# Kernel tuning notes

Measured on AMD Instinct MI355X. Metric: run time of the kernel, lower is better.

Reference implementation:

```python
import jax, jax.numpy as jnp
import numpy as np

BLOCK_SIZE = 64
IN_CHANNELS = 1024
OUT_CHANNELS = 1024
O_NBLOCKS = OUT_CHANNELS // BLOCK_SIZE  # 16
I_NBLOCKS = IN_CHANNELS // BLOCK_SIZE   # 16
N_TOKENS = 32768


def setup_inputs() -> dict:
    key = jax.random.key(0)
    kx, kw = jax.random.split(key)
    x = jax.random.normal(kx, (N_TOKENS, IN_CHANNELS), dtype=jnp.float32)
    # xavier_uniform over the (o_nblocks, i_nblocks, block_size) tensor:
    # fan_in = i_nblocks * block_size, fan_out = block_size (last-dim convention)
    fan_in = I_NBLOCKS * BLOCK_SIZE
    fan_out = BLOCK_SIZE
    limit = float(np.sqrt(6.0 / (fan_in + fan_out)))
    w = jax.random.uniform(kw, (O_NBLOCKS, I_NBLOCKS, BLOCK_SIZE),
                           dtype=jnp.float32, minval=-limit, maxval=limit)
    return {"x": x, "w": w}


def _build_dense_weight(w):
    # w: (R, Q, bs). Dense W[r*bs+i, q*bs+j] = w[r, q, (i - j) mod bs]
    R, Q, bs = w.shape
    i = jnp.arange(bs)
    idx = (i[:, None] - i[None, :]) % bs          # (bs, bs) circulant index
    Wb = w[:, :, idx]                              # (R, Q, bs, bs)
    return Wb.transpose(0, 2, 1, 3).reshape(R * bs, Q * bs)  # (out, in)


def reference(x, w):
    W = _build_dense_weight(w)                     # (out_channels, in_channels)
    return x @ W.T                                 # F.linear, no bias
```

## Files before the change

kernel.cpp:

```cpp
#include <hip/hip_runtime.h>
#include <stdint.h>


#define NTOK 32768
#define NCH  1024
#define BK   64
#define NKT  (NCH / BK)

typedef short bf16x8 __attribute__((ext_vector_type(8)));
typedef float f32x4  __attribute__((ext_vector_type(4)));
typedef unsigned short u16x8 __attribute__((ext_vector_type(8)));

static __device__ __forceinline__ unsigned short f2bf(float f) {
    unsigned int u = __float_as_uint(f);
    u += 0x7FFFu + ((u >> 16) & 1u);
    return (unsigned short)(u >> 16);
}

#define GLOAD16(gp, lp)                                                          \
    __builtin_amdgcn_global_load_lds(                                            \
        (const __attribute__((address_space(1))) unsigned int*)(gp),             \
        (__attribute__((address_space(3))) unsigned int*)(lp), 16, 0, 0)

__global__ void cvt_x_kernel(const float* __restrict__ x, unsigned short* __restrict__ xb) {
    int i = blockIdx.x * blockDim.x + threadIdx.x;
    int row = i >> 7;
    int j   = i & 127;
    const float4* src = (const float4*)(x + (((size_t)row) << 10) + (j << 3));
    float4 a = src[0], b = src[1];
    u16x8 v;
    v[0]=f2bf(a.x); v[1]=f2bf(a.y); v[2]=f2bf(a.z); v[3]=f2bf(a.w);
    v[4]=f2bf(b.x); v[5]=f2bf(b.y); v[6]=f2bf(b.z); v[7]=f2bf(b.w);
    int js = (j & ~7) | ((j & 7) ^ (row & 7));
    *(u16x8*)(xb + (((size_t)row) << 10) + (js << 3)) = v;
}

__global__ void build_w_kernel(const float* __restrict__ w, unsigned short* __restrict__ Wb) {
    int i = blockIdx.x * blockDim.x + threadIdx.x;
    int o = i >> 7;
    int j = i & 127;
    int r = o >> 6;
    int q = j >> 3;
    const float* wrow = w + ((r * 16 + q) << 6);
    int k0 = j << 3;
    u16x8 v;
#pragma unroll
    for (int e = 0; e < 8; ++e) v[e] = f2bf(wrow[(o - (k0 + e)) & 63]);
    int js = (j & ~7) | ((j & 7) ^ (o & 7));
    *(u16x8*)(Wb + (((size_t)o) << 10) + (js << 3)) = v;
}

#define PHASE_BAR() __builtin_amdgcn_s_barrier()
#define LGKM0() asm volatile("s_waitcnt lgkmcnt(0)" ::: "memory")
#define VMCNT0() asm volatile("s_waitcnt vmcnt(0)" ::: "memory")
#define SETPRIO(n) __builtin_amdgcn_s_setprio(n)
#define MFMA4(d, av, bv) d = __builtin_amdgcn_mfma_f32_16x16x32_bf16(av, bv, d, 0, 0, 0)
#define NOHOOK ((void)0)

#define STAGE(bufA, bufB, t) do {                                                \
    const char* _sa = srcA + ((t) << 7);                                         \
    const char* _sb = srcB + ((t) << 7);                                         \
    char* _da = (bufA) + (wv << 10);                                             \
    char* _db = (bufB) + (wv << 10);                                             \
    GLOAD16(_sa, _da); GLOAD16(_sa + (64 << 11), _da + 8192);                    \
    GLOAD16(_sb, _db); GLOAD16(_sb + (64 << 11), _db + 8192);                    \
} while (0)

#define KSTEP(Abuf, Bbuf, DO_STAGE) do {                                         \
    DO_STAGE;                                                                    \
    bf16x8 afr[4][2], bfr[2][2];                                                 \
    _Pragma("unroll") for (int m = 0; m < 4; ++m)                                \
      _Pragma("unroll") for (int ks = 0; ks < 2; ++ks)                           \
        afr[m][ks] = *(const bf16x8*)((Abuf) + a_off[ks] + m * 2048);            \
    _Pragma("unroll") for (int n = 0; n < 2; ++n)                                \
      _Pragma("unroll") for (int ks = 0; ks < 2; ++ks)                           \
        bfr[n][ks] = *(const bf16x8*)((Bbuf) + b_off[ks] + n * 2048);            \
    LGKM0();                                                                     \
    SETPRIO(1);                                                                  \
    _Pragma("unroll") for (int m = 0; m < 4; ++m)                                \
      _Pragma("unroll") for (int n = 0; n < 2; ++n) {                            \
        MFMA4(acc[m][n], afr[m][0], bfr[n][0]);                                  \
        MFMA4(acc[m][n], afr[m][1], bfr[n][1]);                                  \
      }                                                                          \
    SETPRIO(0);                                                                  \
} while (0)

__global__ void __launch_bounds__(512, 4) gemm128_kernel(const unsigned short* __restrict__ A,
                                                         const unsigned short* __restrict__ B,
                                                         float* __restrict__ C) {
    __shared__ __align__(16) char lds[65536];
    char* As0 = lds;
    char* As1 = lds + 16384;
    char* Bs0 = lds + 32768;
    char* Bs1 = lds + 49152;

    int tid  = threadIdx.x;
    int lane = tid & 63;
    int wv   = tid >> 6;
    int wr   = wv >> 2;
    int wc   = wv & 3;

    int cpx = gridDim.x >> 3;
    int wid = ((int)blockIdx.x & 7) * cpx + ((int)blockIdx.x >> 3);
    int tn = wid & 7, tm = wid >> 3;
    int m0 = tm * 128, n0 = tn * 128;

    const char* srcA = (const char*)A + (((size_t)(m0 + (tid >> 3))) << 11) + ((tid & 7) << 4);
    const char* srcB = (const char*)B + (((size_t)(n0 + (tid >> 3))) << 11) + ((tid & 7) << 4);

    int xa   = (lane & 7) << 4;
    int kq16 = (lane >> 4) << 4;
    int abase = (wr * 64 + (lane & 15)) * 128;
    int bbase = (wc * 32 + (lane & 15)) * 128;
    int a_off[2] = { abase + (kq16 ^ xa), abase + ((64 + kq16) ^ xa) };
    int b_off[2] = { bbase + (kq16 ^ xa), bbase + ((64 + kq16) ^ xa) };

    f32x4 acc[4][2] = {};

    STAGE(As0, Bs0, 0);
    VMCNT0(); PHASE_BAR();

    for (int t = 0; t < NKT; t += 2) {
        KSTEP(As0, Bs0, STAGE(As1, Bs1, t + 1));
        VMCNT0(); PHASE_BAR();
        if (t + 2 < NKT) {
            KSTEP(As1, Bs1, STAGE(As0, Bs0, t + 2));
            VMCNT0(); PHASE_BAR();
        } else {
            KSTEP(As1, Bs1, NOHOOK);
        }
    }

    float* Cp = C + ((size_t)(m0 + wr * 64)) * NCH + n0 + wc * 32;
    int cc = lane & 15;
    int rr = (lane >> 4) << 2;
#pragma unroll
    for (int m = 0; m < 4; ++m)
#pragma unroll
        for (int j = 0; j < 4; ++j) {
            float* rowp = Cp + ((size_t)(m * 16 + rr + j)) * NCH;
#pragma unroll
            for (int n = 0; n < 2; ++n)
                rowp[n * 16 + cc] = acc[m][n][j];
        }
}

__global__ void naive_kernel(const float* __restrict__ x, const float* __restrict__ w,
                             float* __restrict__ out) {
    int t = blockIdx.x;
    int o = blockIdx.y * 256 + threadIdx.x;
    const float* xr = x + (size_t)t * NCH;
    int r = o >> 6, oi = o & 63;
    float s = 0.f;
    for (int q = 0; q < 16; ++q) {
        const float* wq = w + (r * 16 + q) * 64;
        const float* xq = xr + q * 64;
#pragma unroll 8
        for (int j = 0; j < 64; ++j) s += xq[j] * wq[(oi - j) & 63];
    }
    out[(size_t)t * NCH + o] = s;
}

extern "C" void kernel_launch(void* const* d_in, const int* in_sizes, int n_in,
                              void* d_out, int out_size, void* d_ws, size_t ws_size,
                              hipStream_t stream) {
    const float* x = (const float*)d_in[0];
    const float* w = (const float*)d_in[1];
    float* out = (float*)d_out;

    const size_t needX = (size_t)NTOK * NCH * sizeof(unsigned short);
    const size_t needW = (size_t)NCH * NCH * sizeof(unsigned short);

    if (ws_size >= needX + needW) {
        unsigned short* xb = (unsigned short*)d_ws;
        unsigned short* Wb = (unsigned short*)((char*)d_ws + needX);
        hipLaunchKernelGGL(cvt_x_kernel, dim3(NTOK * 128 / 256), dim3(256), 0, stream, x, xb);
        hipLaunchKernelGGL(build_w_kernel, dim3(NCH * 128 / 256), dim3(256), 0, stream, w, Wb);
        hipLaunchKernelGGL(gemm128_kernel, dim3(2048), dim3(512), 0, stream, xb, Wb, out);
    } else {
        hipLaunchKernelGGL(naive_kernel, dim3(NTOK, 4), dim3(256), 0, stream, x, w, out);
    }
}
```

Measured before the change: 111.4 us.

## Fuse fp32-to-bf16 conversion of x into the GEMM A-tile loading

Drops the separate conversion pass that wrote a bf16 copy of x. The GEMM now loads fp32 x tiles into registers, converts them to bf16 and writes them to LDS in the swizzled layout, while B still streams directly to LDS. This saves a full read and write pass over the activations, but it doubles the A bytes fetched per tile, and each A tile is re-read by every column tile. The register staging also adds VALU work and vmcnt waits to the main loop.

```diff
diff --git a/kernel.cpp b/kernel.cpp
--- a/kernel.cpp
+++ b/kernel.cpp
@@ -17,23 +17,17 @@
     return (unsigned short)(u >> 16);
 }
 
+static __device__ __forceinline__ u16x8 pack8(float4 a, float4 b) {
+    u16x8 v;
+    v[0]=f2bf(a.x); v[1]=f2bf(a.y); v[2]=f2bf(a.z); v[3]=f2bf(a.w);
+    v[4]=f2bf(b.x); v[5]=f2bf(b.y); v[6]=f2bf(b.z); v[7]=f2bf(b.w);
+    return v;
+}
+
 #define GLOAD16(gp, lp)                                                          \
     __builtin_amdgcn_global_load_lds(                                            \
         (const __attribute__((address_space(1))) unsigned int*)(gp),             \
         (__attribute__((address_space(3))) unsigned int*)(lp), 16, 0, 0)
-
-__global__ void cvt_x_kernel(const float* __restrict__ x, unsigned short* __restrict__ xb) {
-    int i = blockIdx.x * blockDim.x + threadIdx.x;
-    int row = i >> 7;
-    int j   = i & 127;
-    const float4* src = (const float4*)(x + (((size_t)row) << 10) + (j << 3));
-    float4 a = src[0], b = src[1];
-    u16x8 v;
-    v[0]=f2bf(a.x); v[1]=f2bf(a.y); v[2]=f2bf(a.z); v[3]=f2bf(a.w);
-    v[4]=f2bf(b.x); v[5]=f2bf(b.y); v[6]=f2bf(b.z); v[7]=f2bf(b.w);
-    int js = (j & ~7) | ((j & 7) ^ (row & 7));
-    *(u16x8*)(xb + (((size_t)row) << 10) + (js << 3)) = v;
-}
 
 __global__ void build_w_kernel(const float* __restrict__ w, unsigned short* __restrict__ Wb) {
     int i = blockIdx.x * blockDim.x + threadIdx.x;
@@ -52,22 +46,32 @@
 
 #define PHASE_BAR() __builtin_amdgcn_s_barrier()
 #define LGKM0() asm volatile("s_waitcnt lgkmcnt(0)" ::: "memory")
-#define VMCNT0() asm volatile("s_waitcnt vmcnt(0)" ::: "memory")
+#define VMCNT(n) asm volatile("s_waitcnt vmcnt(" #n ")" ::: "memory")
+#define CFENCE() asm volatile("" ::: "memory")
 #define SETPRIO(n) __builtin_amdgcn_s_setprio(n)
 #define MFMA4(d, av, bv) d = __builtin_amdgcn_mfma_f32_16x16x32_bf16(av, bv, d, 0, 0, 0)
-#define NOHOOK ((void)0)
 
-#define STAGE(bufA, bufB, t) do {                                                \
-    const char* _sa = srcA + ((t) << 7);                                         \
-    const char* _sb = srcB + ((t) << 7);                                         \
-    char* _da = (bufA) + (wv << 10);                                             \
-    char* _db = (bufB) + (wv << 10);                                             \
-    GLOAD16(_sa, _da); GLOAD16(_sa + (64 << 11), _da + 8192);                    \
-    GLOAD16(_sb, _db); GLOAD16(_sb + (64 << 11), _db + 8192);                    \
+#define ISSUE_A(t) do {                                                          \
+    const float4* _p = (const float4*)(pA + ((t) << 6));                         \
+    areg[0] = _p[0]; areg[1] = _p[1]; areg[2] = _p[2]; areg[3] = _p[3];          \
+    CFENCE();                                                                    \
 } while (0)
 
-#define KSTEP(Abuf, Bbuf, DO_STAGE) do {                                         \
-    DO_STAGE;                                                                    \
+#define WRITE_A(Abuf) do {                                                       \
+    u16x8 _w0 = pack8(areg[0], areg[1]);                                         \
+    u16x8 _w1 = pack8(areg[2], areg[3]);                                         \
+    *(u16x8*)((Abuf) + aw0) = _w0;                                               \
+    *(u16x8*)((Abuf) + aw1) = _w1;                                               \
+    CFENCE();                                                                    \
+} while (0)
+
+#define STAGE_B(buf, t) do {                                                     \
+    const char* _s = srcB + ((t) << 7);                                          \
+    char* _d = (buf) + (wv << 10);                                               \
+    GLOAD16(_s, _d); GLOAD16(_s + (64 << 11), _d + 8192);                        \
+} while (0)
+
+#define KCOMPUTE(Abuf, Bbuf) do {                                                \
     bf16x8 afr[4][2], bfr[2][2];                                                 \
     _Pragma("unroll") for (int m = 0; m < 4; ++m)                                \
       _Pragma("unroll") for (int ks = 0; ks < 2; ++ks)                           \
@@ -85,9 +89,9 @@
     SETPRIO(0);                                                                  \
 } while (0)
 
-__global__ void __launch_bounds__(512, 4) gemm128_kernel(const unsigned short* __restrict__ A,
-                                                         const unsigned short* __restrict__ B,
-                                                         float* __restrict__ C) {
+__global__ void __launch_bounds__(512, 4) gemm_fused_kernel(const float* __restrict__ X,
+                                                            const unsigned short* __restrict__ B,
+                                                            float* __restrict__ C) {
     __shared__ __align__(16) char lds[65536];
     char* As0 = lds;
     char* As1 = lds + 16384;
@@ -105,7 +109,15 @@
     int tn = wid & 7, tm = wid >> 3;
     int m0 = tm * 128, n0 = tn * 128;
 
-    const char* srcA = (const char*)A + (((size_t)(m0 + (tid >> 3))) << 11) + ((tid & 7) << 4);
+    const float* pA = X + ((size_t)(m0 + (tid >> 2)) << 10) + ((tid & 3) << 4);
+    float4 areg[4];
+
+    int wrow = tid >> 2;
+    int j0   = (tid & 3) << 1;
+    int r7   = wrow & 7;
+    int aw0  = wrow * 128 + (((j0    ) ^ r7) << 4);
+    int aw1  = wrow * 128 + (((j0 + 1) ^ r7) << 4);
+
     const char* srcB = (const char*)B + (((size_t)(n0 + (tid >> 3))) << 11) + ((tid & 7) << 4);
 
     int xa   = (lane & 7) << 4;
@@ -117,17 +129,24 @@
 
     f32x4 acc[4][2] = {};
 
-    STAGE(As0, Bs0, 0);
-    VMCNT0(); PHASE_BAR();
+    ISSUE_A(0); STAGE_B(Bs0, 0);
+    VMCNT(2);
+    WRITE_A(As0);
+    VMCNT(0); LGKM0();
+    PHASE_BAR();
 
     for (int t = 0; t < NKT; t += 2) {
-        KSTEP(As0, Bs0, STAGE(As1, Bs1, t + 1));
-        VMCNT0(); PHASE_BAR();
+        ISSUE_A(t + 1); STAGE_B(Bs1, t + 1);
+        KCOMPUTE(As0, Bs0);
+        VMCNT(2); WRITE_A(As1);
+        VMCNT(0); LGKM0(); PHASE_BAR();
         if (t + 2 < NKT) {
-            KSTEP(As1, Bs1, STAGE(As0, Bs0, t + 2));
-            VMCNT0(); PHASE_BAR();
+            ISSUE_A(t + 2); STAGE_B(Bs0, t + 2);
+            KCOMPUTE(As1, Bs1);
+            VMCNT(2); WRITE_A(As0);
+            VMCNT(0); LGKM0(); PHASE_BAR();
         } else {
-            KSTEP(As1, Bs1, NOHOOK);
+            KCOMPUTE(As1, Bs1);
         }
     }
 
@@ -168,15 +187,12 @@
     const float* w = (const float*)d_in[1];
     float* out = (float*)d_out;
 
-    const size_t needX = (size_t)NTOK * NCH * sizeof(unsigned short);
     const size_t needW = (size_t)NCH * NCH * sizeof(unsigned short);
 
-    if (ws_size >= needX + needW) {
-        unsigned short* xb = (unsigned short*)d_ws;
-        unsigned short* Wb = (unsigned short*)((char*)d_ws + needX);
-        hipLaunchKernelGGL(cvt_x_kernel, dim3(NTOK * 128 / 256), dim3(256), 0, stream, x, xb);
+    if (ws_size >= needW) {
+        unsigned short* Wb = (unsigned short*)d_ws;
         hipLaunchKernelGGL(build_w_kernel, dim3(NCH * 128 / 256), dim3(256), 0, stream, w, Wb);
-        hipLaunchKernelGGL(gemm128_kernel, dim3(2048), dim3(512), 0, stream, xb, Wb, out);
+        hipLaunchKernelGGL(gemm_fused_kernel, dim3(2048), dim3(512), 0, stream, x, Wb, out);
     } else {
         hipLaunchKernelGGL(naive_kernel, dim3(NTOK, 4), dim3(256), 0, stream, x, w, out);
     }
```

New measurement: 115.3 us. 3.5% more time.

## Deepen GEMM LDS pipeline to keep two k-tiles of loads in flight

Applied to the files above, without the earlier changes.

Restructures the main GEMM loop so that two k-tiles are staged ahead. Each step reads its fragments, barriers, then reissues the async global-to-LDS load into the same buffer it just consumed. The step ends with a partial vmcnt wait that only requires the older tile to have landed. This is meant to hide global load latency better than the previous wait-for-all-loads pattern, at the cost of an extra barrier per k-step and a longer unrolled tail.

```diff
diff --git a/kernel.cpp b/kernel.cpp
--- a/kernel.cpp
+++ b/kernel.cpp
@@ -4,8 +4,7 @@
 
 #define NTOK 32768
 #define NCH  1024
-#define BK   64
-#define NKT  (NCH / BK)
+#define NKT  16
 
 typedef short bf16x8 __attribute__((ext_vector_type(8)));
 typedef float f32x4  __attribute__((ext_vector_type(4)));
@@ -50,9 +49,9 @@
     *(u16x8*)(Wb + (((size_t)o) << 10) + (js << 3)) = v;
 }
 
-#define PHASE_BAR() __builtin_amdgcn_s_barrier()
+#define BAR() __builtin_amdgcn_s_barrier()
 #define LGKM0() asm volatile("s_waitcnt lgkmcnt(0)" ::: "memory")
-#define VMCNT0() asm volatile("s_waitcnt vmcnt(0)" ::: "memory")
+#define VMCNT(n) asm volatile("s_waitcnt vmcnt(" #n ")" ::: "memory")
 #define SETPRIO(n) __builtin_amdgcn_s_setprio(n)
 #define MFMA4(d, av, bv) d = __builtin_amdgcn_mfma_f32_16x16x32_bf16(av, bv, d, 0, 0, 0)
 #define NOHOOK ((void)0)
@@ -66,8 +65,7 @@
     GLOAD16(_sb, _db); GLOAD16(_sb + (64 << 11), _db + 8192);                    \
 } while (0)
 
-#define KSTEP(Abuf, Bbuf, DO_STAGE) do {                                         \
-    DO_STAGE;                                                                    \
+#define KSTEP2(Abuf, Bbuf, DO_STAGE, WN) do {                                    \
     bf16x8 afr[4][2], bfr[2][2];                                                 \
     _Pragma("unroll") for (int m = 0; m < 4; ++m)                                \
       _Pragma("unroll") for (int ks = 0; ks < 2; ++ks)                           \
@@ -76,6 +74,8 @@
       _Pragma("unroll") for (int ks = 0; ks < 2; ++ks)                           \
         bfr[n][ks] = *(const bf16x8*)((Bbuf) + b_off[ks] + n * 2048);            \
     LGKM0();                                                                     \
+    BAR();                                                                       \
+    DO_STAGE;                                                                    \
     SETPRIO(1);                                                                  \
     _Pragma("unroll") for (int m = 0; m < 4; ++m)                                \
       _Pragma("unroll") for (int n = 0; n < 2; ++n) {                            \
@@ -83,6 +83,8 @@
         MFMA4(acc[m][n], afr[m][1], bfr[n][1]);                                  \
       }                                                                          \
     SETPRIO(0);                                                                  \
+    WN;                                                                          \
+    BAR();                                                                       \
 } while (0)
 
 __global__ void __launch_bounds__(512, 4) gemm128_kernel(const unsigned short* __restrict__ A,
@@ -118,17 +120,38 @@
     f32x4 acc[4][2] = {};
 
     STAGE(As0, Bs0, 0);
-    VMCNT0(); PHASE_BAR();
-
-    for (int t = 0; t < NKT; t += 2) {
-        KSTEP(As0, Bs0, STAGE(As1, Bs1, t + 1));
-        VMCNT0(); PHASE_BAR();
-        if (t + 2 < NKT) {
-            KSTEP(As1, Bs1, STAGE(As0, Bs0, t + 2));
-            VMCNT0(); PHASE_BAR();
-        } else {
-            KSTEP(As1, Bs1, NOHOOK);
-        }
+    STAGE(As1, Bs1, 1);
+    VMCNT(4); BAR();
+
+    for (int t = 0; t < 12; t += 2) {
+        KSTEP2(As0, Bs0, STAGE(As0, Bs0, t + 2), VMCNT(4));
+        KSTEP2(As1, Bs1, STAGE(As1, Bs1, t + 3), VMCNT(4));
+    }
+    KSTEP2(As0, Bs0, STAGE(As0, Bs0, 14), VMCNT(4));
+    KSTEP2(As1, Bs1, STAGE(As1, Bs1, 15), VMCNT(4));
+    KSTEP2(As0, Bs0, NOHOOK, VMCNT(0));
+    {
+        bf16x8 afr[4][2], bfr[2][2];
+#pragma unroll
+        for (int m = 0; m < 4; ++m)
+#pragma unroll
+            for (int ks = 0; ks < 2; ++ks)
+                afr[m][ks] = *(const bf16x8*)(As1 + a_off[ks] + m * 2048);
+#pragma unroll
+        for (int n = 0; n < 2; ++n)
+#pragma unroll
+            for (int ks = 0; ks < 2; ++ks)
+                bfr[n][ks] = *(const bf16x8*)(Bs1 + b_off[ks] + n * 2048);
+        LGKM0();
+        SETPRIO(1);
+#pragma unroll
+        for (int m = 0; m < 4; ++m)
+#pragma unroll
+            for (int n = 0; n < 2; ++n) {
+                MFMA4(acc[m][n], afr[m][0], bfr[n][0]);
+                MFMA4(acc[m][n], afr[m][1], bfr[n][1]);
+            }
+        SETPRIO(0);
     }
 
     float* Cp = C + ((size_t)(m0 + wr * 64)) * NCH + n0 + wc * 32;
```

After: 109.5 us. No clear change (-1.7%).

## Load B fragments directly from global into registers, dropping B LDS staging

Applied to the files above, without the earlier changes.

The GEMM now fetches the weight (B) fragments straight from global memory into double-buffered registers instead of staging them through LDS. LDS use is halved and the B-side LDS reads are removed, with the weight matrix stored unswizzled so the direct loads line up. This trades LDS traffic and footprint for more global/L2 loads per wave, since each wave row duplicates B fetches, and for higher register pressure.

```diff
diff --git a/kernel.cpp b/kernel.cpp
--- a/kernel.cpp
+++ b/kernel.cpp
@@ -4,8 +4,7 @@
 
 #define NTOK 32768
 #define NCH  1024
-#define BK   64
-#define NKT  (NCH / BK)
+#define NKT  16
 
 typedef short bf16x8 __attribute__((ext_vector_type(8)));
 typedef float f32x4  __attribute__((ext_vector_type(4)));
@@ -46,41 +45,42 @@
     u16x8 v;
 #pragma unroll
     for (int e = 0; e < 8; ++e) v[e] = f2bf(wrow[(o - (k0 + e)) & 63]);
-    int js = (j & ~7) | ((j & 7) ^ (o & 7));
-    *(u16x8*)(Wb + (((size_t)o) << 10) + (js << 3)) = v;
+    *(u16x8*)(Wb + (((size_t)o) << 10) + (j << 3)) = v;
 }
 
-#define PHASE_BAR() __builtin_amdgcn_s_barrier()
+#define BAR() __builtin_amdgcn_s_barrier()
 #define LGKM0() asm volatile("s_waitcnt lgkmcnt(0)" ::: "memory")
 #define VMCNT0() asm volatile("s_waitcnt vmcnt(0)" ::: "memory")
 #define SETPRIO(n) __builtin_amdgcn_s_setprio(n)
 #define MFMA4(d, av, bv) d = __builtin_amdgcn_mfma_f32_16x16x32_bf16(av, bv, d, 0, 0, 0)
 #define NOHOOK ((void)0)
 
-#define STAGE(bufA, bufB, t) do {                                                \
+#define STAGE_A(buf, t) do {                                                     \
     const char* _sa = srcA + ((t) << 7);                                         \
-    const char* _sb = srcB + ((t) << 7);                                         \
-    char* _da = (bufA) + (wv << 10);                                             \
-    char* _db = (bufB) + (wv << 10);                                             \
+    char* _da = (buf) + (wv << 10);                                              \
     GLOAD16(_sa, _da); GLOAD16(_sa + (64 << 11), _da + 8192);                    \
-    GLOAD16(_sb, _db); GLOAD16(_sb + (64 << 11), _db + 8192);                    \
 } while (0)
 
-#define KSTEP(Abuf, Bbuf, DO_STAGE) do {                                         \
-    DO_STAGE;                                                                    \
-    bf16x8 afr[4][2], bfr[2][2];                                                 \
+#define ISSUE_B(bank, t) do {                                                    \
+    const char* _b = pB + ((t) << 7);                                            \
+    bank[0][0] = *(const bf16x8*)(_b);                                           \
+    bank[0][1] = *(const bf16x8*)(_b + 64);                                      \
+    bank[1][0] = *(const bf16x8*)(_b + 32768);                                   \
+    bank[1][1] = *(const bf16x8*)(_b + 32768 + 64);                              \
+} while (0)
+
+#define KSTEP(Abuf, bC, HOOKS) do {                                              \
+    HOOKS;                                                                       \
+    bf16x8 afr[4][2];                                                            \
     _Pragma("unroll") for (int m = 0; m < 4; ++m)                                \
       _Pragma("unroll") for (int ks = 0; ks < 2; ++ks)                           \
         afr[m][ks] = *(const bf16x8*)((Abuf) + a_off[ks] + m * 2048);            \
-    _Pragma("unroll") for (int n = 0; n < 2; ++n)                                \
-      _Pragma("unroll") for (int ks = 0; ks < 2; ++ks)                           \
-        bfr[n][ks] = *(const bf16x8*)((Bbuf) + b_off[ks] + n * 2048);            \
     LGKM0();                                                                     \
     SETPRIO(1);                                                                  \
     _Pragma("unroll") for (int m = 0; m < 4; ++m)                                \
       _Pragma("unroll") for (int n = 0; n < 2; ++n) {                            \
-        MFMA4(acc[m][n], afr[m][0], bfr[n][0]);                                  \
-        MFMA4(acc[m][n], afr[m][1], bfr[n][1]);                                  \
+        MFMA4(acc[m][n], afr[m][0], bC[n][0]);                                   \
+        MFMA4(acc[m][n], afr[m][1], bC[n][1]);                                   \
       }                                                                          \
     SETPRIO(0);                                                                  \
 } while (0)
@@ -88,11 +88,9 @@
 __global__ void __launch_bounds__(512, 4) gemm128_kernel(const unsigned short* __restrict__ A,
                                                          const unsigned short* __restrict__ B,
                                                          float* __restrict__ C) {
-    __shared__ __align__(16) char lds[65536];
+    __shared__ __align__(16) char lds[32768];
     char* As0 = lds;
     char* As1 = lds + 16384;
-    char* Bs0 = lds + 32768;
-    char* Bs1 = lds + 49152;
 
     int tid  = threadIdx.x;
     int lane = tid & 63;
@@ -106,28 +104,30 @@
     int m0 = tm * 128, n0 = tn * 128;
 
     const char* srcA = (const char*)A + (((size_t)(m0 + (tid >> 3))) << 11) + ((tid & 7) << 4);
-    const char* srcB = (const char*)B + (((size_t)(n0 + (tid >> 3))) << 11) + ((tid & 7) << 4);
+
+    const char* pB = (const char*)B + (((size_t)(n0 + wc * 32 + (lane & 15))) << 11)
+                     + ((lane >> 4) << 4);
+    bf16x8 bE[2][2], bO[2][2];
 
     int xa   = (lane & 7) << 4;
     int kq16 = (lane >> 4) << 4;
     int abase = (wr * 64 + (lane & 15)) * 128;
-    int bbase = (wc * 32 + (lane & 15)) * 128;
     int a_off[2] = { abase + (kq16 ^ xa), abase + ((64 + kq16) ^ xa) };
-    int b_off[2] = { bbase + (kq16 ^ xa), bbase + ((64 + kq16) ^ xa) };
 
     f32x4 acc[4][2] = {};
 
-    STAGE(As0, Bs0, 0);
-    VMCNT0(); PHASE_BAR();
+    ISSUE_B(bE, 0);
+    STAGE_A(As0, 0);
+    VMCNT0(); BAR();
 
     for (int t = 0; t < NKT; t += 2) {
-        KSTEP(As0, Bs0, STAGE(As1, Bs1, t + 1));
-        VMCNT0(); PHASE_BAR();
+        KSTEP(As0, bE, { STAGE_A(As1, t + 1); ISSUE_B(bO, t + 1); });
+        VMCNT0(); BAR();
         if (t + 2 < NKT) {
-            KSTEP(As1, Bs1, STAGE(As0, Bs0, t + 2));
-            VMCNT0(); PHASE_BAR();
+            KSTEP(As1, bO, { STAGE_A(As0, t + 2); ISSUE_B(bE, t + 2); });
+            VMCNT0(); BAR();
         } else {
-            KSTEP(As1, Bs1, NOHOOK);
+            KSTEP(As1, bO, NOHOOK);
         }
     }
 
```

Measured after the change: 184.8 us. 1.66x slower.
